# Performance work log

Hardware: AMD Instinct MI355X
Metric: run time of the kernel (lower is better)

Reference implementation:

```python
import jax, jax.numpy as jnp
import numpy as np

N, IN, H, D, OUT = 2048, 256, 12, 32, 384
ALPHA = 0.2


def setup_inputs() -> dict:
    key = jax.random.key(0)
    ks = jax.random.split(key, 12)
    s = 0.05
    return {
        "x": jax.random.normal(ks[0], (N, IN), jnp.float32),
        "adj": jax.random.uniform(ks[1], (N, N), jnp.float32),  # all > 0 -> fully connected mask
        "W": jax.random.normal(ks[2], (H * D, IN), jnp.float32) * s,
        "attn_src": jax.random.normal(ks[3], (H, D), jnp.float32) * s,
        "attn_dst": jax.random.normal(ks[4], (H, D), jnp.float32) * s,
        "edge_W": jax.random.normal(ks[5], (H, 1), jnp.float32) * s,
        "edge_b": jax.random.normal(ks[6], (H,), jnp.float32) * s,
        "res_W": jax.random.normal(ks[7], (H * D, IN), jnp.float32) * s,
        "res_b": jax.random.normal(ks[8], (H * D,), jnp.float32) * s,
        "fus_W": jax.random.normal(ks[9], (OUT, H * D), jnp.float32) * s,
        "fus_b": jax.random.normal(ks[10], (OUT,), jnp.float32) * s,
    }


def reference(x, adj, W, attn_src, attn_dst, edge_W, edge_b, res_W, res_b, fus_W, fus_b):
    n = x.shape[0]
    h = (x @ W.T).reshape(n, H, D)                      # [N,H,D]
    a_src = jnp.einsum("nhd,hd->nh", h, attn_src)       # [N,H]
    a_dst = jnp.einsum("nhd,hd->nh", h, attn_dst)       # [N,H]
    attn = a_src[:, None, :] + a_dst[None, :, :]        # [N,N,H]
    # edge_encoder: Linear(1 -> H) applied to adj[...,None]
    attn = attn + adj[..., None] * edge_W.reshape(1, 1, H) + edge_b
    mask = (adj > 0)[..., None]                         # [N,N,1]
    attn = jnp.where(mask, attn, -jnp.inf)
    attn = jnp.where(attn >= 0, attn, ALPHA * attn)     # leaky_relu
    attn = jax.nn.softmax(attn, axis=1)                 # over source nodes j
    # dropout is identity in eval mode
    h_out = jnp.einsum("ijh,jhd->ihd", attn, h).reshape(n, H * D)
    h_out = h_out + x @ res_W.T + res_b                 # residual
    out = jax.nn.gelu(h_out @ fus_W.T + fus_b, approximate=False)
    return out
```

## Files before the change

### kernel.cpp

```cpp
#include <hip/hip_runtime.h>
#include <hip/hip_bf16.h>

#define NN 2048
#define NH 12
#define HD 32
#define CALL 384

typedef float f32x16 __attribute__((ext_vector_type(16)));
typedef _Float16 f16x4 __attribute__((ext_vector_type(4)));

static __device__ __forceinline__ f32x16 mfma8f16(f16x4 a, f16x4 b, f32x16 c) {
    return __builtin_amdgcn_mfma_f32_32x32x8f16(a, b, c, 0, 0, 0);
}
static __device__ __forceinline__ f16x4 u2f(uint2 u) {
    union { uint2 u2; f16x4 f; } c; c.u2 = u; return c.f;
}

__global__ __launch_bounds__(512) void gemm01(
    const float* __restrict__ A, const float* __restrict__ B0,
    const float* __restrict__ B1, const float* __restrict__ bias1,
    const float* __restrict__ attn_src, const float* __restrict__ attn_dst,
    _Float16* __restrict__ outT, float* __restrict__ outF,
    float* __restrict__ asrc, float* __restrict__ adstT)
{
    __shared__ __align__(16) char smem[17408];
    _Float16 (*As)[68] = (_Float16(*)[68])(smem);
    _Float16 (*Bs)[68] = (_Float16(*)[68])(smem + 8704);
    float* red = (float*)smem;

    const int t = threadIdx.x;
    const int w = t >> 6, l = t & 63, g = l >> 5, il = l & 31;
    const int q = w & 3, kg = w >> 2;
    const int m0 = blockIdx.x * 64, n0 = blockIdx.y * 64;
    const int mode = blockIdx.z;
    const float* B = mode ? B1 : B0;
    const int wr = (q >> 1) * 32, wc = (q & 1) * 32;
    const int ti = t >> 3, seg = t & 7;
    const int Kdim = 256;

    f32x16 acc;
#pragma unroll
    for (int r = 0; r < 16; ++r) acc[r] = 0.f;

#pragma unroll 1
    for (int ss = 0; ss < 4; ++ss) {
        const int kk = ss * 64;
        __syncthreads();
        {
            const float* Ap = A + (size_t)(m0 + ti) * Kdim + kk + seg * 8;
            float4 v0 = *reinterpret_cast<const float4*>(Ap);
            float4 v1 = *reinterpret_cast<const float4*>(Ap + 4);
            f16x4 lo = {(_Float16)v0.x, (_Float16)v0.y, (_Float16)v0.z, (_Float16)v0.w};
            f16x4 hi = {(_Float16)v1.x, (_Float16)v1.y, (_Float16)v1.z, (_Float16)v1.w};
            *reinterpret_cast<f16x4*>(&As[ti][seg * 8])     = lo;
            *reinterpret_cast<f16x4*>(&As[ti][seg * 8 + 4]) = hi;
        }
        {
            const float* Bp = B + (size_t)(n0 + ti) * Kdim + kk + seg * 8;
            float4 v0 = *reinterpret_cast<const float4*>(Bp);
            float4 v1 = *reinterpret_cast<const float4*>(Bp + 4);
            f16x4 lo = {(_Float16)v0.x, (_Float16)v0.y, (_Float16)v0.z, (_Float16)v0.w};
            f16x4 hi = {(_Float16)v1.x, (_Float16)v1.y, (_Float16)v1.z, (_Float16)v1.w};
            *reinterpret_cast<f16x4*>(&Bs[ti][seg * 8])     = lo;
            *reinterpret_cast<f16x4*>(&Bs[ti][seg * 8 + 4]) = hi;
        }
        __syncthreads();
#pragma unroll
        for (int kc = 0; kc < 4; ++kc) {
            f16x4 af = *reinterpret_cast<const f16x4*>(&As[wr + il][kg * 32 + kc * 8 + 4 * g]);
            f16x4 bf = *reinterpret_cast<const f16x4*>(&Bs[wc + il][kg * 32 + kc * 8 + 4 * g]);
            acc = mfma8f16(af, bf, acc);
        }
    }

    __syncthreads();
    if (kg == 1) {
#pragma unroll
        for (int r = 0; r < 16; ++r) red[(q * 16 + r) * 64 + l] = acc[r];
    }
    __syncthreads();
    if (kg != 0) return;
#pragma unroll
    for (int r = 0; r < 16; ++r) acc[r] += red[(q * 16 + r) * 64 + l];

    const int colg = n0 + wc + il;
    if (mode == 0) {
#pragma unroll
        for (int p = 0; p < 4; ++p) {
            const int row = m0 + wr + 8 * p + 4 * g;
            f16x4 v;
#pragma unroll
            for (int r = 0; r < 4; ++r) v[r] = (_Float16)acc[4 * p + r];
            *reinterpret_cast<f16x4*>(&outT[(size_t)colg * NN + row]) = v;
        }
        const int hstar = colg >> 5;
        const float sv = attn_src[hstar * HD + il];
        const float dv = attn_dst[hstar * HD + il];
        float ps[16], pd[16];
#pragma unroll
        for (int r = 0; r < 16; ++r) { ps[r] = acc[r] * sv; pd[r] = acc[r] * dv; }
#pragma unroll
        for (int m = 1; m <= 16; m <<= 1) {
#pragma unroll
            for (int r = 0; r < 16; ++r) {
                ps[r] += __shfl_xor(ps[r], m);
                pd[r] += __shfl_xor(pd[r], m);
            }
        }
        if (il == 0) {
#pragma unroll
            for (int r = 0; r < 16; ++r) {
                const int row = m0 + wr + (r & 3) + 8 * (r >> 2) + 4 * g;
                asrc[row * NH + hstar] = ps[r];
                adstT[(size_t)hstar * NN + row] = pd[r] * 1.44269504089f;
            }
        }
    } else {
        const float bs = bias1[colg];
#pragma unroll
        for (int r = 0; r < 16; ++r) {
            const int row = m0 + wr + (r & 3) + 8 * (r >> 2) + 4 * g;
            outF[(size_t)row * CALL + colg] = acc[r] + bs;
        }
    }
}

__global__ __launch_bounds__(512) void gemm2(
    const _Float16* __restrict__ A16, const float* __restrict__ B,
    const float* __restrict__ bias, float* __restrict__ outF)
{
    __shared__ __align__(16) char smem[17408];
    _Float16 (*As)[68] = (_Float16(*)[68])(smem);
    _Float16 (*Bs)[68] = (_Float16(*)[68])(smem + 8704);
    float* red = (float*)smem;

    const int t = threadIdx.x;
    const int w = t >> 6, l = t & 63, g = l >> 5, il = l & 31;
    const int q = w & 3, kg = w >> 2;
    const int m0 = blockIdx.x * 64, n0 = blockIdx.y * 64;
    const int wr = (q >> 1) * 32, wc = (q & 1) * 32;
    const int ti = t >> 3, seg = t & 7;
    const int Kdim = 384;

    f32x16 acc;
#pragma unroll
    for (int r = 0; r < 16; ++r) acc[r] = 0.f;

#pragma unroll 1
    for (int ss = 0; ss < 6; ++ss) {
        const int kk = ss * 64;
        __syncthreads();
        {
            const uint4 v = *reinterpret_cast<const uint4*>(A16 + (size_t)(m0 + ti) * Kdim + kk + seg * 8);
            *reinterpret_cast<uint2*>(&As[ti][seg * 8])     = make_uint2(v.x, v.y);
            *reinterpret_cast<uint2*>(&As[ti][seg * 8 + 4]) = make_uint2(v.z, v.w);
        }
        {
            const float* Bp = B + (size_t)(n0 + ti) * Kdim + kk + seg * 8;
            float4 v0 = *reinterpret_cast<const float4*>(Bp);
            float4 v1 = *reinterpret_cast<const float4*>(Bp + 4);
            f16x4 lo = {(_Float16)v0.x, (_Float16)v0.y, (_Float16)v0.z, (_Float16)v0.w};
            f16x4 hi = {(_Float16)v1.x, (_Float16)v1.y, (_Float16)v1.z, (_Float16)v1.w};
            *reinterpret_cast<f16x4*>(&Bs[ti][seg * 8])     = lo;
            *reinterpret_cast<f16x4*>(&Bs[ti][seg * 8 + 4]) = hi;
        }
        __syncthreads();
#pragma unroll
        for (int kc = 0; kc < 4; ++kc) {
            f16x4 af = *reinterpret_cast<const f16x4*>(&As[wr + il][kg * 32 + kc * 8 + 4 * g]);
            f16x4 bf = *reinterpret_cast<const f16x4*>(&Bs[wc + il][kg * 32 + kc * 8 + 4 * g]);
            acc = mfma8f16(af, bf, acc);
        }
    }

    __syncthreads();
    if (kg == 1) {
#pragma unroll
        for (int r = 0; r < 16; ++r) red[(q * 16 + r) * 64 + l] = acc[r];
    }
    __syncthreads();
    if (kg != 0) return;
#pragma unroll
    for (int r = 0; r < 16; ++r) acc[r] += red[(q * 16 + r) * 64 + l];

    const int colg = n0 + wc + il;
    const float bs = bias[colg];
#pragma unroll
    for (int r = 0; r < 16; ++r) {
        const int row = m0 + wr + (r & 3) + 8 * (r >> 2) + 4 * g;
        float vv = acc[r] + bs;
        vv = 0.5f * vv * (1.0f + erff(vv * 0.70710678118f));
        outF[(size_t)row * CALL + colg] = vv;
    }
}

__global__ __launch_bounds__(1024, 4) void attn10(
    const float* __restrict__ adj, const _Float16* __restrict__ hT,
    const float* __restrict__ asrc, const float* __restrict__ adstT,
    const float* __restrict__ eW, const float* __restrict__ eb,
    const float* __restrict__ res, _Float16* __restrict__ hsum)
{
    __shared__ __align__(16) char smem[55296];
    const int t = threadIdx.x;
    const int w = t >> 6, l = t & 63, g = l >> 5, il = l & 31;
    const int band = blockIdx.x & 63, hg = blockIdx.x >> 6;
    const int i0 = band * 32, h0 = hg * 3, c0 = hg * 96;

    float* adst_s = (float*)(smem + w * 1536);
    float* red    = (float*)smem;
    float* dsum_s = (float*)(smem + 49152);

    const float LOG2E = 1.44269504089f;
    float base_h[3], eWr[3];
#pragma unroll
    for (int hh = 0; hh < 3; ++hh) {
        base_h[hh] = (asrc[(size_t)(i0 + il) * NH + h0 + hh] + eb[h0 + hh]) * LOG2E;
        eWr[hh] = eW[h0 + hh] * LOG2E;
    }

    const int jbase = w * 128;
#pragma unroll
    for (int p = 0; p < 6; ++p) {
        const int idx = p * 64 + l;
        adst_s[idx] = adstT[(size_t)(h0 + (idx >> 7)) * NN + jbase + (idx & 127)];
    }

    f32x16 acc[3];
#pragma unroll
    for (int hh = 0; hh < 3; ++hh)
#pragma unroll
        for (int r = 0; r < 16; ++r) acc[hh][r] = 0.f;
    float dsum[3] = {0.f, 0.f, 0.f};

    const _Float16* hbase = hT  + (size_t)(c0 + il) * NN + jbase + 16 * g;
    const float*    abase = adj + (size_t)(i0 + il) * NN + jbase + 16 * g;

#pragma unroll 1
    for (int tl = 0; tl < 4; ++tl) {
        const int jo = tl * 32;
        float4 aj0 = *reinterpret_cast<const float4*>(abase + jo);
        float4 aj1 = *reinterpret_cast<const float4*>(abase + jo + 4);
        float4 aj2 = *reinterpret_cast<const float4*>(abase + jo + 8);
        float4 aj3 = *reinterpret_cast<const float4*>(abase + jo + 12);
#pragma unroll
        for (int hh = 0; hh < 3; ++hh) {
            const _Float16* hp = hbase + (size_t)(hh * 32) * NN + jo;
            const uint4 hA = *reinterpret_cast<const uint4*>(hp);
            const uint4 hB = *reinterpret_cast<const uint4*>(hp + 8);
#pragma unroll
            for (int ks = 0; ks < 4; ++ks) {
                const float4 a4 = (ks == 0) ? aj0 : (ks == 1) ? aj1 : (ks == 2) ? aj2 : aj3;
                const float4 ad = *reinterpret_cast<const float4*>(
                    &adst_s[hh * 128 + jo + 16 * g + 4 * ks]);
                f16x4 ef;
#pragma unroll
                for (int jj = 0; jj < 4; ++jj) {
                    const float ajv = (&a4.x)[jj];
                    float tt = fmaf(ajv, eWr[hh], base_h[hh] + (&ad.x)[jj]);
                    tt = fmaxf(tt, 0.2f * tt);
                    const float ee = ajv > 0.f ? __builtin_amdgcn_exp2f(tt) : 0.f;
                    dsum[hh] += ee;
                    ef[jj] = (_Float16)ee;
                }
                const uint2 hu = (ks == 0) ? make_uint2(hA.x, hA.y)
                               : (ks == 1) ? make_uint2(hA.z, hA.w)
                               : (ks == 2) ? make_uint2(hB.x, hB.y)
                                           : make_uint2(hB.z, hB.w);
                acc[hh] = mfma8f16(ef, u2f(hu), acc[hh]);
            }
        }
    }

    __syncthreads();
#pragma unroll
    for (int hh = 0; hh < 3; ++hh) {
        const float dtot = dsum[hh] + __shfl_xor(dsum[hh], 32);
        if (g == 0) dsum_s[(w * 3 + hh) * 32 + il] = dtot;
    }
    if (w < 4) {
#pragma unroll
        for (int hh = 0; hh < 3; ++hh)
#pragma unroll
            for (int reg = 0; reg < 16; ++reg)
                red[((w * 3 + hh) * 16 + reg) * 64 + l] = acc[hh][reg];
    }
    __syncthreads();
    if (w >= 4 && w < 8) {
#pragma unroll
        for (int hh = 0; hh < 3; ++hh)
#pragma unroll
            for (int reg = 0; reg < 16; ++reg)
                red[(((w - 4) * 3 + hh) * 16 + reg) * 64 + l] += acc[hh][reg];
    }
    __syncthreads();
    if (w >= 8 && w < 12) {
#pragma unroll
        for (int hh = 0; hh < 3; ++hh)
#pragma unroll
            for (int reg = 0; reg < 16; ++reg)
                red[(((w - 8) * 3 + hh) * 16 + reg) * 64 + l] += acc[hh][reg];
    }
    __syncthreads();
    if (w >= 12) {
#pragma unroll
        for (int hh = 0; hh < 3; ++hh)
#pragma unroll
            for (int reg = 0; reg < 16; ++reg)
                red[(((w - 12) * 3 + hh) * 16 + reg) * 64 + l] += acc[hh][reg];
    }
    __syncthreads();

    {
        const int reg = w;
        const int row_off = (reg & 3) + 8 * (reg >> 2) + 4 * g;
        const int row = i0 + row_off;
#pragma unroll
        for (int hh = 0; hh < 3; ++hh) {
            float v = 0.f, d = 0.f;
#pragma unroll
            for (int p = 0; p < 4; ++p)
                v += red[((p * 3 + hh) * 16 + reg) * 64 + l];
#pragma unroll
            for (int ww = 0; ww < 16; ++ww)
                d += dsum_s[(ww * 3 + hh) * 32 + row_off];
            const int col = (h0 + hh) * 32 + il;
            hsum[(size_t)row * CALL + col] = (_Float16)(v / d + res[(size_t)row * CALL + col]);
        }
    }
}

extern "C" void kernel_launch(void* const* d_in, const int* in_sizes, int n_in,
                              void* d_out, int out_size, void* d_ws, size_t ws_size,
                              hipStream_t stream)
{
    const float* x        = (const float*)d_in[0];
    const float* adj      = (const float*)d_in[1];
    const float* W        = (const float*)d_in[2];
    const float* attn_src = (const float*)d_in[3];
    const float* attn_dst = (const float*)d_in[4];
    const float* edge_W   = (const float*)d_in[5];
    const float* edge_b   = (const float*)d_in[6];
    const float* res_W    = (const float*)d_in[7];
    const float* res_b    = (const float*)d_in[8];
    const float* fus_W    = (const float*)d_in[9];
    const float* fus_b    = (const float*)d_in[10];
    float* out = (float*)d_out;

    char* ws = (char*)d_ws;
    size_t off = 0;
    auto alloc = [&](size_t bytes) { void* p = ws + off; off = (off + bytes + 255) & ~(size_t)255; return p; };
    _Float16* hT    = (_Float16*)alloc((size_t)CALL * NN * 2);
    float*    res   = (float*)alloc((size_t)NN * CALL * 4);
    float*    asrc  = (float*)alloc((size_t)NN * NH * 4);
    float*    adstT = (float*)alloc((size_t)NH * NN * 4);
    _Float16* hsum  = (_Float16*)alloc((size_t)NN * CALL * 2);
    (void)ws_size;

    gemm01<<<dim3(32, 6, 2), dim3(512), 0, stream>>>(x, W, res_W, res_b, attn_src, attn_dst, hT, res, asrc, adstT);
    attn10<<<256, dim3(1024), 0, stream>>>(adj, hT, asrc, adstT, edge_W, edge_b, res, hsum);
    gemm2<<<dim3(32, 6), dim3(512), 0, stream>>>(hsum, fus_W, fus_b, out);
}
```

Baseline: 52.81 us.

## Halve attention block width, double per-wave key range, and software-pipeline adj loads

The attention kernel now runs 512 threads (8 waves) per block instead of 1024, so each wave covers 256 source nodes rather than 128. The main loop is fully unrolled with double-buffered adj register loads, so the next tile's adj reads are issued while the current tile's exp and MFMA work runs. The denominator accumulates into four separate partial sums to shorten the dependency chain. The cross-wave reduction needs fewer barrier stages and each wave writes two output rows. The cost is more registers per thread and fewer waves available to hide latency.

```diff
diff --git a/kernel.cpp b/kernel.cpp
--- a/kernel.cpp
+++ b/kernel.cpp
@@ -194,19 +194,19 @@
     }
 }
 
-__global__ __launch_bounds__(1024, 4) void attn10(
+__global__ __launch_bounds__(512, 2) void attn12(
     const float* __restrict__ adj, const _Float16* __restrict__ hT,
     const float* __restrict__ asrc, const float* __restrict__ adstT,
     const float* __restrict__ eW, const float* __restrict__ eb,
     const float* __restrict__ res, _Float16* __restrict__ hsum)
 {
-    __shared__ __align__(16) char smem[55296];
+    __shared__ __align__(16) char smem[52224];
     const int t = threadIdx.x;
     const int w = t >> 6, l = t & 63, g = l >> 5, il = l & 31;
     const int band = blockIdx.x & 63, hg = blockIdx.x >> 6;
     const int i0 = band * 32, h0 = hg * 3, c0 = hg * 96;
 
-    float* adst_s = (float*)(smem + w * 1536);
+    float* adst_s = (float*)(smem + w * 3072);
     float* red    = (float*)smem;
     float* dsum_s = (float*)(smem + 49152);
 
@@ -218,11 +218,11 @@
         eWr[hh] = eW[h0 + hh] * LOG2E;
     }
 
-    const int jbase = w * 128;
-#pragma unroll
-    for (int p = 0; p < 6; ++p) {
+    const int jbase = w * 256;
+#pragma unroll
+    for (int p = 0; p < 12; ++p) {
         const int idx = p * 64 + l;
-        adst_s[idx] = adstT[(size_t)(h0 + (idx >> 7)) * NN + jbase + (idx & 127)];
+        adst_s[idx] = adstT[(size_t)(h0 + (idx >> 8)) * NN + jbase + (idx & 255)];
     }
 
     f32x16 acc[3];
@@ -230,51 +230,74 @@
     for (int hh = 0; hh < 3; ++hh)
 #pragma unroll
         for (int r = 0; r < 16; ++r) acc[hh][r] = 0.f;
-    float dsum[3] = {0.f, 0.f, 0.f};
+    float4 dsumv[3];
+#pragma unroll
+    for (int hh = 0; hh < 3; ++hh) dsumv[hh] = make_float4(0.f, 0.f, 0.f, 0.f);
 
     const _Float16* hbase = hT  + (size_t)(c0 + il) * NN + jbase + 16 * g;
     const float*    abase = adj + (size_t)(i0 + il) * NN + jbase + 16 * g;
 
-#pragma unroll 1
-    for (int tl = 0; tl < 4; ++tl) {
-        const int jo = tl * 32;
-        float4 aj0 = *reinterpret_cast<const float4*>(abase + jo);
-        float4 aj1 = *reinterpret_cast<const float4*>(abase + jo + 4);
-        float4 aj2 = *reinterpret_cast<const float4*>(abase + jo + 8);
-        float4 aj3 = *reinterpret_cast<const float4*>(abase + jo + 12);
-#pragma unroll
-        for (int hh = 0; hh < 3; ++hh) {
-            const _Float16* hp = hbase + (size_t)(hh * 32) * NN + jo;
-            const uint4 hA = *reinterpret_cast<const uint4*>(hp);
-            const uint4 hB = *reinterpret_cast<const uint4*>(hp + 8);
-#pragma unroll
-            for (int ks = 0; ks < 4; ++ks) {
-                const float4 a4 = (ks == 0) ? aj0 : (ks == 1) ? aj1 : (ks == 2) ? aj2 : aj3;
-                const float4 ad = *reinterpret_cast<const float4*>(
-                    &adst_s[hh * 128 + jo + 16 * g + 4 * ks]);
-                f16x4 ef;
-#pragma unroll
-                for (int jj = 0; jj < 4; ++jj) {
-                    const float ajv = (&a4.x)[jj];
-                    float tt = fmaf(ajv, eWr[hh], base_h[hh] + (&ad.x)[jj]);
-                    tt = fmaxf(tt, 0.2f * tt);
-                    const float ee = ajv > 0.f ? __builtin_amdgcn_exp2f(tt) : 0.f;
-                    dsum[hh] += ee;
-                    ef[jj] = (_Float16)ee;
-                }
-                const uint2 hu = (ks == 0) ? make_uint2(hA.x, hA.y)
-                               : (ks == 1) ? make_uint2(hA.z, hA.w)
-                               : (ks == 2) ? make_uint2(hB.x, hB.y)
-                                           : make_uint2(hB.z, hB.w);
-                acc[hh] = mfma8f16(ef, u2f(hu), acc[hh]);
-            }
-        }
-    }
+    float4 ajA0, ajA1, ajA2, ajA3, ajB0, ajB1, ajB2, ajB3;
+
+#define LOADADJ(B0_, B1_, B2_, B3_, JO)                                        \
+    B0_ = *reinterpret_cast<const float4*>(abase + (JO));                      \
+    B1_ = *reinterpret_cast<const float4*>(abase + (JO) + 4);                  \
+    B2_ = *reinterpret_cast<const float4*>(abase + (JO) + 8);                  \
+    B3_ = *reinterpret_cast<const float4*>(abase + (JO) + 12);
+
+#define TILE(B0_, B1_, B2_, B3_, JO)                                           \
+    {                                                                          \
+        uint4 hA[3], hB[3];                                                    \
+        _Pragma("unroll")                                                      \
+        for (int hh = 0; hh < 3; ++hh) {                                       \
+            const _Float16* hp = hbase + (size_t)(hh * 32) * NN + (JO);        \
+            hA[hh] = *reinterpret_cast<const uint4*>(hp);                      \
+            hB[hh] = *reinterpret_cast<const uint4*>(hp + 8);                  \
+        }                                                                      \
+        _Pragma("unroll")                                                      \
+        for (int hh = 0; hh < 3; ++hh) {                                       \
+            _Pragma("unroll")                                                  \
+            for (int ks = 0; ks < 4; ++ks) {                                   \
+                const float4 a4 = (ks == 0) ? B0_ : (ks == 1) ? B1_            \
+                                : (ks == 2) ? B2_ : B3_;                       \
+                const float4 ad = *reinterpret_cast<const float4*>(            \
+                    &adst_s[hh * 256 + (JO) + 16 * g + 4 * ks]);               \
+                f16x4 ef;                                                      \
+                _Pragma("unroll")                                              \
+                for (int jj = 0; jj < 4; ++jj) {                               \
+                    const float ajv = (&a4.x)[jj];                             \
+                    float tt = fmaf(ajv, eWr[hh], base_h[hh] + (&ad.x)[jj]);   \
+                    tt = fmaxf(tt, 0.2f * tt);                                 \
+                    const float ee = ajv > 0.f ? __builtin_amdgcn_exp2f(tt) : 0.f; \
+                    (&dsumv[hh].x)[jj] += ee;                                  \
+                    ef[jj] = (_Float16)ee;                                     \
+                }                                                              \
+                const uint2 hu = (ks == 0) ? make_uint2(hA[hh].x, hA[hh].y)    \
+                               : (ks == 1) ? make_uint2(hA[hh].z, hA[hh].w)    \
+                               : (ks == 2) ? make_uint2(hB[hh].x, hB[hh].y)    \
+                                           : make_uint2(hB[hh].z, hB[hh].w);   \
+                acc[hh] = mfma8f16(ef, u2f(hu), acc[hh]);                      \
+            }                                                                  \
+        }                                                                      \
+    }
+
+    LOADADJ(ajA0, ajA1, ajA2, ajA3, 0);
+    LOADADJ(ajB0, ajB1, ajB2, ajB3, 32);   TILE(ajA0, ajA1, ajA2, ajA3, 0);
+    LOADADJ(ajA0, ajA1, ajA2, ajA3, 64);   TILE(ajB0, ajB1, ajB2, ajB3, 32);
+    LOADADJ(ajB0, ajB1, ajB2, ajB3, 96);   TILE(ajA0, ajA1, ajA2, ajA3, 64);
+    LOADADJ(ajA0, ajA1, ajA2, ajA3, 128);  TILE(ajB0, ajB1, ajB2, ajB3, 96);
+    LOADADJ(ajB0, ajB1, ajB2, ajB3, 160);  TILE(ajA0, ajA1, ajA2, ajA3, 128);
+    LOADADJ(ajA0, ajA1, ajA2, ajA3, 192);  TILE(ajB0, ajB1, ajB2, ajB3, 160);
+    LOADADJ(ajB0, ajB1, ajB2, ajB3, 224);  TILE(ajA0, ajA1, ajA2, ajA3, 192);
+                                           TILE(ajB0, ajB1, ajB2, ajB3, 224);
+#undef LOADADJ
+#undef TILE
 
     __syncthreads();
 #pragma unroll
     for (int hh = 0; hh < 3; ++hh) {
-        const float dtot = dsum[hh] + __shfl_xor(dsum[hh], 32);
+        const float ds = (dsumv[hh].x + dsumv[hh].y) + (dsumv[hh].z + dsumv[hh].w);
+        const float dtot = ds + __shfl_xor(ds, 32);
         if (g == 0) dsum_s[(w * 3 + hh) * 32 + il] = dtot;
     }
     if (w < 4) {
@@ -285,7 +308,7 @@
                 red[((w * 3 + hh) * 16 + reg) * 64 + l] = acc[hh][reg];
     }
     __syncthreads();
-    if (w >= 4 && w < 8) {
+    if (w >= 4) {
 #pragma unroll
         for (int hh = 0; hh < 3; ++hh)
 #pragma unroll
@@ -293,25 +316,10 @@
                 red[(((w - 4) * 3 + hh) * 16 + reg) * 64 + l] += acc[hh][reg];
     }
     __syncthreads();
-    if (w >= 8 && w < 12) {
-#pragma unroll
-        for (int hh = 0; hh < 3; ++hh)
-#pragma unroll
-            for (int reg = 0; reg < 16; ++reg)
-                red[(((w - 8) * 3 + hh) * 16 + reg) * 64 + l] += acc[hh][reg];
-    }
-    __syncthreads();
-    if (w >= 12) {
-#pragma unroll
-        for (int hh = 0; hh < 3; ++hh)
-#pragma unroll
-            for (int reg = 0; reg < 16; ++reg)
-                red[(((w - 12) * 3 + hh) * 16 + reg) * 64 + l] += acc[hh][reg];
-    }
-    __syncthreads();
-
-    {
-        const int reg = w;
+
+#pragma unroll
+    for (int rr = 0; rr < 2; ++rr) {
+        const int reg = w + rr * 8;
         const int row_off = (reg & 3) + 8 * (reg >> 2) + 4 * g;
         const int row = i0 + row_off;
 #pragma unroll
@@ -321,7 +329,7 @@
             for (int p = 0; p < 4; ++p)
                 v += red[((p * 3 + hh) * 16 + reg) * 64 + l];
 #pragma unroll
-            for (int ww = 0; ww < 16; ++ww)
+            for (int ww = 0; ww < 8; ++ww)
                 d += dsum_s[(ww * 3 + hh) * 32 + row_off];
             const int col = (h0 + hh) * 32 + il;
             hsum[(size_t)row * CALL + col] = (_Float16)(v / d + res[(size_t)row * CALL + col]);
@@ -357,6 +365,6 @@
     (void)ws_size;
 
     gemm01<<<dim3(32, 6, 2), dim3(512), 0, stream>>>(x, W, res_W, res_b, attn_src, attn_dst, hT, res, asrc, adstT);
-    attn10<<<256, dim3(1024), 0, stream>>>(adj, hT, asrc, adstT, edge_W, edge_b, res, hsum);
+    attn12<<<256, dim3(512), 0, stream>>>(adj, hT, asrc, adstT, edge_W, edge_b, res, hsum);
     gemm2<<<dim3(32, 6), dim3(512), 0, stream>>>(hsum, fus_W, fus_b, out);
 }
```

Measured after the change: 71.76 us. 1.36x slower.
